# Optimization experiments

Hardware: AMD Instinct MI355X
Metric: run time of the kernel (lower is better)

Reference implementation:

```python
import jax, jax.numpy as jnp
import numpy as np

N = 50000        # nodes
E = 1_600_000    # edges
D_IN = 128       # input_dim
H = 2            # n_heads
C = 32           # out_dim per head


def setup_inputs() -> dict:
    key = jax.random.key(0)
    ks = jax.random.split(key, 10)
    x = jax.random.normal(ks[0], (N, D_IN), dtype=jnp.float32)
    edge_index = jax.random.randint(ks[1], (2, E), 0, N, dtype=jnp.int64)
    s = 1.0 / np.sqrt(D_IN)
    Wq = jax.random.uniform(ks[2], (D_IN, H * C), jnp.float32, -s, s)
    bq = jax.random.uniform(ks[3], (H * C,), jnp.float32, -s, s)
    Wk = jax.random.uniform(ks[4], (D_IN, H * C), jnp.float32, -s, s)
    bk = jax.random.uniform(ks[5], (H * C,), jnp.float32, -s, s)
    Wv = jax.random.uniform(ks[6], (D_IN, H * C), jnp.float32, -s, s)
    bv = jax.random.uniform(ks[7], (H * C,), jnp.float32, -s, s)
    Wskip = jax.random.uniform(ks[8], (D_IN, H * C), jnp.float32, -s, s)
    bskip = jax.random.uniform(ks[9], (H * C,), jnp.float32, -s, s)
    return {"x": x, "edge_index": edge_index, "Wq": Wq, "bq": bq,
            "Wk": Wk, "bk": bk, "Wv": Wv, "bv": bv,
            "Wskip": Wskip, "bskip": bskip}


def reference(x, edge_index, Wq, bq, Wk, bk, Wv, bv, Wskip, bskip):
    # IntraGraphAttention.forward: ELU then TransformerConv (PyG semantics,
    # concat=True, root_weight=True, beta=False).
    x = jax.nn.elu(x)
    src, dst = edge_index[0], edge_index[1]

    q = (x @ Wq + bq).reshape(N, H, C)   # queries at target nodes
    k = (x @ Wk + bk).reshape(N, H, C)   # keys at source nodes
    v = (x @ Wv + bv).reshape(N, H, C)   # values at source nodes

    # per-edge attention logits [E, H]
    alpha = jnp.einsum('ehc,ehc->eh', q[dst], k[src]) / np.sqrt(C).astype(np.float32)

    # segment softmax over incoming edges of each target node
    m = jax.ops.segment_max(alpha, dst, num_segments=N)            # [N, H]
    m = jnp.where(jnp.isfinite(m), m, 0.0)                          # empty segments
    ex = jnp.exp(alpha - m[dst])                                    # [E, H]
    denom = jax.ops.segment_sum(ex, dst, num_segments=N)            # [N, H]
    w = ex / jnp.maximum(denom[dst], 1e-16)                         # [E, H]

    # weighted scatter-add of values to targets
    msg = v[src] * w[:, :, None]                                    # [E, H, C]
    out = jax.ops.segment_sum(msg, dst, num_segments=N)             # [N, H, C]
    out = out.reshape(N, H * C)

    # root/skip connection
    return out + x @ Wskip + bskip
```

## Files before the change

kernel.cpp:

```cpp
#include <hip/hip_runtime.h>
#include <hip/hip_bf16.h>


#define DIN 128
#define HC  64
#define EPB 4096
#define CAPB 12288
#define CAPQ 3072

typedef _Float16 h2 __attribute__((ext_vector_type(2)));
typedef _Float16 h4 __attribute__((ext_vector_type(4)));
typedef _Float16 h8 __attribute__((ext_vector_type(8)));
typedef float    f4 __attribute__((ext_vector_type(4)));
typedef float    f2v __attribute__((ext_vector_type(2)));

#if defined(__has_builtin)
#if __has_builtin(__builtin_amdgcn_fdot2)
#define HAVE_FDOT2 1
#endif
#endif

static __device__ __forceinline__ float fdot2(h2 a, h2 b, float c) {
#ifdef HAVE_FDOT2
    return __builtin_amdgcn_fdot2(a, b, c, false);
#else
    return fmaf((float)a.x, (float)b.x, fmaf((float)a.y, (float)b.y, c));
#endif
}

__global__ __launch_bounds__(256) void k_prep(
        const float* __restrict__ Wq, const float* __restrict__ Wk,
        const float* __restrict__ Wv, const float* __restrict__ Ws,
        _Float16* __restrict__ Wh, int* __restrict__ bucketCnt) {
    int t = threadIdx.x;
    if (blockIdx.x == 0) bucketCnt[t] = 0;
    int idx = blockIdx.x * 256 + t;
    int m    = idx >> 13;
    int rem  = idx & 8191;
    int grp  = rem >> 9;
    int ks   = grp >> 2;
    int nt   = grp & 3;
    int r3   = rem & 511;
    int lane = r3 >> 3;
    int j    = r3 & 7;
    int k = ks * 32 + (lane >> 4) * 8 + j;
    int n = nt * 16 + (lane & 15);
    const float* W = (m == 0) ? Wq : (m == 1) ? Wk : (m == 2) ? Wv : Ws;
    Wh[idx] = (_Float16)W[k * 64 + n];
}

#define TB 32
#define XS 136
__global__ __launch_bounds__(256) void k_fused(
        const float4* __restrict__ x4,
        const _Float16* __restrict__ Wh,
        const float* __restrict__ bq, const float* __restrict__ bk,
        const float* __restrict__ bv, const float* __restrict__ bs,
        _Float16* __restrict__ Q, unsigned char* __restrict__ K8,
        unsigned char* __restrict__ V8,
        float* __restrict__ OUT, int N,
        const int* __restrict__ ei, int* __restrict__ bucketCnt,
        unsigned int* __restrict__ part, int E, int qb) {
    __shared__ alignas(16) char smem[4096 + EPB * 4];
    int t = threadIdx.x;

    if ((int)blockIdx.x >= qb) {
        int* hist  = (int*)smem;
        int* lbase = hist + 256;
        int* cur   = lbase + 256;
        int* gbase = cur + 256;
        unsigned int* stg = (unsigned int*)(smem + 4096);

        int e0 = (blockIdx.x - qb) * EPB;
        int cnt = min(EPB, E - e0);
        hist[t] = 0; cur[t] = 0;
        __syncthreads();

        unsigned int pk[EPB / 256];
        #pragma unroll
        for (int u = 0; u < EPB / 256; ++u) {
            int i = t + u * 256;
            if (i < cnt) {
                unsigned int d = (unsigned int)ei[E + e0 + i];
                unsigned int s = (unsigned int)ei[e0 + i];
                pk[u] = (d << 16) | s;
                atomicAdd(&hist[d >> 8], 1);
            }
        }
        __syncthreads();
        {
            int v = hist[t];
            lbase[t] = v;
            __syncthreads();
            for (int off = 1; off < 256; off <<= 1) {
                int xv = (t >= off) ? lbase[t - off] : 0;
                __syncthreads();
                lbase[t] += xv;
                __syncthreads();
            }
            int incl = lbase[t];
            __syncthreads();
            lbase[t] = incl - v;
        }
        {
            int c = hist[t];
            if (c > 0) gbase[t] = t * CAPB + atomicAdd(&bucketCnt[t], c);
        }
        __syncthreads();
        #pragma unroll
        for (int u = 0; u < EPB / 256; ++u) {
            int i = t + u * 256;
            if (i < cnt) {
                int b = pk[u] >> 24;
                int r = atomicAdd(&cur[b], 1);
                stg[lbase[b] + r] = pk[u];
            }
        }
        __syncthreads();
        for (int i = t; i < cnt; i += 256) {
            unsigned int pkv = stg[i];
            int b = pkv >> 24;
            part[gbase[b] + (i - lbase[b])] = pkv;
        }
        return;
    }

    _Float16* xs = (_Float16*)smem;
    int n0 = blockIdx.x * TB;

    #pragma unroll
    for (int u = 0; u < 4; ++u) {
        int idx = t + u * 256;
        int row = idx >> 5;
        int k4  = idx & 31;
        int node = n0 + row;
        float4 v = make_float4(0.f, 0.f, 0.f, 0.f);
        if (node < N) v = x4[(size_t)node * 32 + k4];
        v.x = (v.x > 0.f) ? v.x : (__expf(v.x) - 1.0f);
        v.y = (v.y > 0.f) ? v.y : (__expf(v.y) - 1.0f);
        v.z = (v.z > 0.f) ? v.z : (__expf(v.z) - 1.0f);
        v.w = (v.w > 0.f) ? v.w : (__expf(v.w) - 1.0f);
        h4 hv = { (_Float16)v.x, (_Float16)v.y, (_Float16)v.z, (_Float16)v.w };
        *(h4*)&xs[row * XS + k4 * 4] = hv;
    }
    __syncthreads();

    int m    = t >> 6;
    int lane = t & 63;
    int lr   = lane & 15;
    int lq   = lane >> 4;

    const _Float16* Wm = Wh + m * 8192;
    const float* bias = (m == 0) ? bq : (m == 1) ? bk : (m == 2) ? bv : bs;

    f4 acc[2][4];
    #pragma unroll
    for (int mt = 0; mt < 2; ++mt)
        #pragma unroll
        for (int nt = 0; nt < 4; ++nt)
            acc[mt][nt] = (f4){0.f, 0.f, 0.f, 0.f};

    #pragma unroll
    for (int ks = 0; ks < 4; ++ks) {
        h8 a0 = *(const h8*)&xs[lr * XS + ks * 32 + lq * 8];
        h8 a1 = *(const h8*)&xs[(16 + lr) * XS + ks * 32 + lq * 8];
        #pragma unroll
        for (int nt = 0; nt < 4; ++nt) {
            h8 b = *(const h8*)&Wm[((ks * 4 + nt) << 9) + lane * 8];
            acc[0][nt] = __builtin_amdgcn_mfma_f32_16x16x32_f16(a0, b, acc[0][nt], 0, 0, 0);
            acc[1][nt] = __builtin_amdgcn_mfma_f32_16x16x32_f16(a1, b, acc[1][nt], 0, 0, 0);
        }
    }

    #pragma unroll
    for (int nt = 0; nt < 4; ++nt) {
        int col = nt * 16 + lr;
        float bb = bias[col];
        #pragma unroll
        for (int mt = 0; mt < 2; ++mt) {
            #pragma unroll
            for (int r = 0; r < 4; ++r) {
                int node = n0 + mt * 16 + lq * 4 + r;
                if (node < N) {
                    float val = acc[mt][nt][r] + bb;
                    if (m == 3) {
                        OUT[((size_t)node << 6) + col] = val;
                    } else if (m == 0) {
                        Q[((size_t)node << 6) + col] = (_Float16)val;
                    } else {
                        unsigned char* O8 = (m == 1) ? K8 : V8;
                        int pk8 = __builtin_amdgcn_cvt_pk_fp8_f32(val, val, 0, false);
                        O8[((size_t)node << 6) + col] = (unsigned char)(pk8 & 0xFF);
                    }
                }
            }
        }
    }
}

__global__ __launch_bounds__(512) void k_build(
        const unsigned int* __restrict__ part, const int* __restrict__ bucketCnt,
        unsigned short* __restrict__ srcs16, int* __restrict__ row_ptr,
        int N, int NBK, int E) {
    __shared__ int hist[256], basep[256], cur[64], sd[256];
    __shared__ unsigned short sbuf[CAPQ];
    __shared__ int s_outBase, s_cnt;
    int t = threadIdx.x;
    int bqid = blockIdx.x;
    int b = bqid >> 2;
    int h = bqid & 3;

    int bc = (t < NBK) ? bucketCnt[t] : 0;
    if (t < 256) sd[t] = bc;
    __syncthreads();
    for (int off = 1; off < 256; off <<= 1) {
        int xv = (t >= off && t < 256) ? sd[t - off] : 0;
        __syncthreads();
        if (t < 256) sd[t] += xv;
        __syncthreads();
    }
    if (t == b) { s_outBase = sd[t] - bc; s_cnt = bc; }
    if (bqid == 0 && t == 256) row_ptr[N] = E;
    if (t < 256) hist[t] = 0;
    if (t < 64) cur[t] = 0;
    __syncthreads();
    int outBase = s_outBase;
    int cnt = min(s_cnt, CAPB);
    int s0 = b * CAPB;

    for (int i = t; i < cnt; i += 512) {
        atomicAdd(&hist[(part[s0 + i] >> 16) & 255], 1);
    }
    __syncthreads();
    {
        int v = (t < 256) ? hist[t] : 0;
        if (t < 256) sd[t] = v;
        __syncthreads();
        for (int off = 1; off < 256; off <<= 1) {
            int xv = (t >= off && t < 256) ? sd[t - off] : 0;
            __syncthreads();
            if (t < 256) sd[t] += xv;
            __syncthreads();
        }
        if (t < 256) basep[t] = sd[t] - v;
    }
    __syncthreads();

    int lo = h << 6;
    int base0 = basep[lo];
    int qcnt = ((h == 3) ? cnt : basep[lo + 64]) - base0;

    for (int i = t; i < cnt; i += 512) {
        unsigned int pkv = part[s0 + i];
        int d = (pkv >> 16) & 255;
        if ((d >> 6) == h) {
            int r = atomicAdd(&cur[d - lo], 1);
            int pos = basep[d] - base0 + r;
            if (pos < CAPQ) sbuf[pos] = (unsigned short)(pkv & 0xFFFFu);
        }
    }
    __syncthreads();
    for (int i = t; i < qcnt && i < CAPQ; i += 512)
        srcs16[outBase + base0 + i] = sbuf[i];

    int node = (b << 8) + lo + t;
    if (t < 64 && node < N) row_ptr[node] = outBase + basep[lo + t];
}

__global__ __launch_bounds__(256) void k_attn(
        const _Float16* __restrict__ Q, const unsigned char* __restrict__ K8,
        const unsigned char* __restrict__ V8, const int* __restrict__ row_ptr,
        const unsigned short* __restrict__ srcs16, float* __restrict__ out, int N) {
    int lane = threadIdx.x & 63;
    int wave = threadIdx.x >> 6;
    int n = blockIdx.x * 4 + wave;
    if (n >= N) return;
    int h5 = lane & 32;
    int c  = lane & 31;
    int pairHalf = (lane >> 4) & 1;
    int clg = (h5 >> 1) + (lane & 15);

    int start = row_ptr[n];
    int deg   = row_ptr[n + 1] - start;
    if (deg <= 0) return;

    h8 q8[4];
    {
        const h8* qp = (const h8*)(Q + ((size_t)n << 6) + h5);
        #pragma unroll
        for (int r = 0; r < 4; ++r) q8[r] = qp[r];
    }
    const h2* q2 = (const h2*)q8;

    const float scale = 0.17677669529663687f;
    float lsum = 0.f;
    float2 acc2 = make_float2(0.f, 0.f);

    int sc_next = (c < deg) ? (int)srcs16[start + c] : 0;

    for (int i0 = 0; i0 < deg; i0 += 32) {
        int nb = min(32, deg - i0);
        int sc = sc_next;

        const unsigned char* kp = K8 + ((size_t)sc << 6) + h5;
        uint4 ka = *(const uint4*)kp;
        uint4 kb = *(const uint4*)(kp + 16);

        int i1 = i0 + 32;
        if (i1 < deg) {
            sc_next = (c < deg - i1) ? (int)srcs16[start + i1 + c] : 0;
        }

        float s = 0.f;
#define KDOT(kw, idx) { \
        f2v f01 = __builtin_amdgcn_cvt_pk_f32_fp8((int)(kw), false); \
        f2v f23 = __builtin_amdgcn_cvt_pk_f32_fp8((int)(kw), true);  \
        auto p01 = __builtin_amdgcn_cvt_pkrtz(f01[0], f01[1]); \
        auto p23 = __builtin_amdgcn_cvt_pkrtz(f23[0], f23[1]); \
        s = fdot2(*(h2*)&p01, q2[2*(idx)],   s); \
        s = fdot2(*(h2*)&p23, q2[2*(idx)+1], s); }
        KDOT(ka.x, 0) KDOT(ka.y, 1) KDOT(ka.z, 2) KDOT(ka.w, 3)
        KDOT(kb.x, 4) KDOT(kb.y, 5) KDOT(kb.z, 6) KDOT(kb.w, 7)
#undef KDOT
        float ex = (c < nb) ? __expf(s * scale) : 0.f;
        lsum += ex;

        int nbp = (nb + 7) & ~7;
        for (int j0 = 0; j0 < nbp; j0 += 8) {
            #pragma unroll
            for (int u = 0; u < 4; ++u) {
                int j = j0 + 2 * u + pairHalf;
                float w  = __shfl(ex, h5 + j, 64);
                int   sj = __shfl(sc, h5 + j, 64);
                unsigned short vw = *(const unsigned short*)
                    (V8 + ((size_t)sj << 6) + (clg << 1));
                f2v vf = __builtin_amdgcn_cvt_pk_f32_fp8((int)vw, false);
                acc2.x = fmaf(w, vf[0], acc2.x);
                acc2.y = fmaf(w, vf[1], acc2.y);
            }
        }
    }

    acc2.x += __shfl_xor(acc2.x, 16, 64);
    acc2.y += __shfl_xor(acc2.y, 16, 64);

    float ls = lsum;
    ls += __shfl_xor(ls, 16, 64);
    ls += __shfl_xor(ls,  8, 64);
    ls += __shfl_xor(ls,  4, 64);
    ls += __shfl_xor(ls,  2, 64);
    ls += __shfl_xor(ls,  1, 64);
    float rden = 1.0f / fmaxf(ls, 1e-16f);

    if ((lane & 16) == 0) {
        float2* o2 = (float2*)out + ((size_t)n << 5) + clg;
        float2 cur2 = *o2;
        cur2.x += acc2.x * rden;
        cur2.y += acc2.y * rden;
        *o2 = cur2;
    }
}

extern "C" void kernel_launch(void* const* d_in, const int* in_sizes, int n_in,
                              void* d_out, int out_size, void* d_ws, size_t ws_size,
                              hipStream_t stream) {
    const float* x  = (const float*)d_in[0];
    const int*   ei = (const int*)d_in[1];
    const float* Wq = (const float*)d_in[2];
    const float* bq = (const float*)d_in[3];
    const float* Wk = (const float*)d_in[4];
    const float* bk = (const float*)d_in[5];
    const float* Wv = (const float*)d_in[6];
    const float* bv = (const float*)d_in[7];
    const float* Ws = (const float*)d_in[8];
    const float* bs = (const float*)d_in[9];
    float* out = (float*)d_out;

    int N = in_sizes[0] / DIN;
    int E = in_sizes[1] / 2;
    int NBK = (N + 255) >> 8;

    char* ws = (char*)d_ws;
    size_t off = 0;
    auto carve = [&](size_t bytes) -> void* {
        void* p = ws + off;
        off = (off + bytes + 255) & ~(size_t)255;
        return p;
    };
    int*            bucketCnt = (int*)carve(256 * sizeof(int));
    int*            row_ptr   = (int*)carve((size_t)(N + 1) * sizeof(int));
    unsigned int*   part      = (unsigned int*)carve((size_t)NBK * CAPB * sizeof(unsigned int));
    unsigned short* srcs16    = (unsigned short*)carve((size_t)E * sizeof(unsigned short));
    _Float16*       Wh        = (_Float16*)carve(4 * 8192 * sizeof(_Float16));
    _Float16*       Qh        = (_Float16*)carve((size_t)N * HC * sizeof(_Float16));
    unsigned char*  K8        = (unsigned char*)carve((size_t)N * HC);
    unsigned char*  V8        = (unsigned char*)carve((size_t)N * HC);
    (void)ws_size; (void)n_in; (void)out_size;

    int qb = (N + TB - 1) / TB;
    int cb = (E + EPB - 1) / EPB;

    k_prep<<<128, 256, 0, stream>>>(Wq, Wk, Wv, Ws, Wh, bucketCnt);
    k_fused<<<qb + cb, 256, 0, stream>>>(
        (const float4*)x, Wh, bq, bk, bv, bs,
        Qh, K8, V8, out, N,
        ei, bucketCnt, part, E, qb);
    k_build<<<4 * NBK, 512, 0, stream>>>(part, bucketCnt, srcs16, row_ptr, N, NBK, E);
    k_attn<<<(N + 3) / 4, 256, 0, stream>>>(Qh, K8, V8, row_ptr, srcs16, out, N);
}
```

Measured before the change: 178.4 us.

## Interleave K and V fp8 rows per node and prefetch next K chunk

K and V fp8 projections are stored in one interleaved 128-byte row per node instead of two separate arrays, so the K gather and the later V gather for the same source node land in the same cache line region. The attention loop also loads the next chunk's K vectors right after the current logits are computed, overlapping that gather latency with the V accumulation loop. This costs extra registers for the prefetched K data and a somewhat larger stride in the per-node layout.

```diff
diff --git a/kernel.cpp b/kernel.cpp
--- a/kernel.cpp
+++ b/kernel.cpp
@@ -56,8 +56,7 @@
         const _Float16* __restrict__ Wh,
         const float* __restrict__ bq, const float* __restrict__ bk,
         const float* __restrict__ bv, const float* __restrict__ bs,
-        _Float16* __restrict__ Q, unsigned char* __restrict__ K8,
-        unsigned char* __restrict__ V8,
+        _Float16* __restrict__ Q, unsigned char* __restrict__ KV8,
         float* __restrict__ OUT, int N,
         const int* __restrict__ ei, int* __restrict__ bucketCnt,
         unsigned int* __restrict__ part, int E, int qb) {
@@ -188,9 +187,9 @@
                     } else if (m == 0) {
                         Q[((size_t)node << 6) + col] = (_Float16)val;
                     } else {
-                        unsigned char* O8 = (m == 1) ? K8 : V8;
                         int pk8 = __builtin_amdgcn_cvt_pk_fp8_f32(val, val, 0, false);
-                        O8[((size_t)node << 6) + col] = (unsigned char)(pk8 & 0xFF);
+                        KV8[((size_t)node << 7) + ((m == 2) ? 64 : 0) + col] =
+                            (unsigned char)(pk8 & 0xFF);
                     }
                 }
             }
@@ -268,8 +267,8 @@
 }
 
 __global__ __launch_bounds__(256) void k_attn(
-        const _Float16* __restrict__ Q, const unsigned char* __restrict__ K8,
-        const unsigned char* __restrict__ V8, const int* __restrict__ row_ptr,
+        const _Float16* __restrict__ Q, const unsigned char* __restrict__ KV8,
+        const int* __restrict__ row_ptr,
         const unsigned short* __restrict__ srcs16, float* __restrict__ out, int N) {
     int lane = threadIdx.x & 63;
     int wave = threadIdx.x >> 6;
@@ -296,20 +295,21 @@
     float lsum = 0.f;
     float2 acc2 = make_float2(0.f, 0.f);
 
-    int sc_next = (c < deg) ? (int)srcs16[start + c] : 0;
+    int sc_cur = (c < deg) ? (int)srcs16[start + c] : 0;
+    uint4 ka, kb;
+    {
+        const unsigned char* kp = KV8 + ((size_t)sc_cur << 7) + h5;
+        ka = *(const uint4*)kp;
+        kb = *(const uint4*)(kp + 16);
+    }
 
     for (int i0 = 0; i0 < deg; i0 += 32) {
         int nb = min(32, deg - i0);
-        int sc = sc_next;
-
-        const unsigned char* kp = K8 + ((size_t)sc << 6) + h5;
-        uint4 ka = *(const uint4*)kp;
-        uint4 kb = *(const uint4*)(kp + 16);
-
+        int sc = sc_cur;
         int i1 = i0 + 32;
-        if (i1 < deg) {
-            sc_next = (c < deg - i1) ? (int)srcs16[start + i1 + c] : 0;
-        }
+
+        int sc_next = 0;
+        if (i1 < deg && c < deg - i1) sc_next = (int)srcs16[start + i1 + c];
 
         float s = 0.f;
 #define KDOT(kw, idx) { \
@@ -325,6 +325,13 @@
         float ex = (c < nb) ? __expf(s * scale) : 0.f;
         lsum += ex;
 
+        if (i1 < deg) {
+            const unsigned char* kpn = KV8 + ((size_t)sc_next << 7) + h5;
+            ka = *(const uint4*)kpn;
+            kb = *(const uint4*)(kpn + 16);
+        }
+        sc_cur = sc_next;
+
         int nbp = (nb + 7) & ~7;
         for (int j0 = 0; j0 < nbp; j0 += 8) {
             #pragma unroll
@@ -333,7 +340,7 @@
                 float w  = __shfl(ex, h5 + j, 64);
                 int   sj = __shfl(sc, h5 + j, 64);
                 unsigned short vw = *(const unsigned short*)
-                    (V8 + ((size_t)sj << 6) + (clg << 1));
+                    (KV8 + ((size_t)sj << 7) + 64 + (clg << 1));
                 f2v vf = __builtin_amdgcn_cvt_pk_f32_fp8((int)vw, false);
                 acc2.x = fmaf(w, vf[0], acc2.x);
                 acc2.y = fmaf(w, vf[1], acc2.y);
@@ -393,8 +400,7 @@
     unsigned short* srcs16    = (unsigned short*)carve((size_t)E * sizeof(unsigned short));
     _Float16*       Wh        = (_Float16*)carve(4 * 8192 * sizeof(_Float16));
     _Float16*       Qh        = (_Float16*)carve((size_t)N * HC * sizeof(_Float16));
-    unsigned char*  K8        = (unsigned char*)carve((size_t)N * HC);
-    unsigned char*  V8        = (unsigned char*)carve((size_t)N * HC);
+    unsigned char*  KV8       = (unsigned char*)carve((size_t)N * 128);
     (void)ws_size; (void)n_in; (void)out_size;
 
     int qb = (N + TB - 1) / TB;
@@ -403,8 +409,8 @@
     k_prep<<<128, 256, 0, stream>>>(Wq, Wk, Wv, Ws, Wh, bucketCnt);
     k_fused<<<qb + cb, 256, 0, stream>>>(
         (const float4*)x, Wh, bq, bk, bv, bs,
-        Qh, K8, V8, out, N,
+        Qh, KV8, out, N,
         ei, bucketCnt, part, E, qb);
     k_build<<<4 * NBK, 512, 0, stream>>>(part, bucketCnt, srcs16, row_ptr, N, NBK, E);
-    k_attn<<<(N + 3) / 4, 256, 0, stream>>>(Qh, K8, V8, row_ptr, srcs16, out, N);
-}
+    k_attn<<<(N + 3) / 4, 256, 0, stream>>>(Qh, KV8, row_ptr, srcs16, out, N);
+}
```

Result: no change. 177.8 us (-0.3%).
